# Optimization experiments

Hardware: AMD Instinct MI355X
Metric: run time of the kernel (lower is better)

The kernel has to match this reference:

```python
import jax, jax.numpy as jnp
import numpy as np

SIGMA = 32.0

def setup_inputs() -> dict:
    key = jax.random.key(0)
    k1, k2, k3 = jax.random.split(key, 3)
    N = 128
    W = 1024
    L = 1024
    init_vectors = jax.random.normal(k1, (2, N), dtype=jnp.float32) / 32.0
    x_coord = jax.random.randint(k2, (N,), 0, W, dtype=jnp.int64)
    y_coord = jax.random.randint(k3, (N,), 0, L, dtype=jnp.int64)
    return {
        "init_vectors": init_vectors,
        "x_coord": x_coord,
        "y_coord": y_coord,
        "width": W,
        "lenth": L,
    }

def reference(init_vectors, x_coord, y_coord, width, lenth):
    # Per-pixel Gaussian RBF voting:
    #   field[0, c, x, y] = sum_n exp(-((x-xc_n)^2 + (y-yc_n)^2) / (2*sigma^2)) * v[c, n]
    inv_two_sigma2 = 1.0 / (2.0 * SIGMA * SIGMA)
    xs = jnp.arange(width, dtype=jnp.float32)
    ys = jnp.arange(lenth, dtype=jnp.float32)
    xc = x_coord.astype(jnp.float32)
    yc = y_coord.astype(jnp.float32)
    dx2 = (xs[:, None] - xc[None, :]) ** 2  # [W, N]
    dy2 = (ys[:, None] - yc[None, :]) ** 2  # [L, N]
    # weights: [W, L, N]
    w = jnp.exp(-(dx2[:, None, :] + dy2[None, :, :]) * inv_two_sigma2)
    # contract over vectors -> [2, W, L]
    field = jnp.einsum("xyn,cn->cxy", w, init_vectors)
    return field[None]  # [1, 2, W, L]
```

## Files before the change

kernel.cpp:

```cpp
#include <hip/hip_runtime.h>


constexpr int N = 128;
constexpr int W = 1024;
constexpr int L = 1024;
constexpr float SIGMA = 32.0f;

constexpr int TX = 8;
constexpr int THREADS = 256;
constexpr int TY = THREADS;

__global__ __launch_bounds__(THREADS)
void rbf_field_kernel(const float* __restrict__ v,
                      const int*   __restrict__ xc,
                      const int*   __restrict__ yc,
                      float*       __restrict__ out)
{
    __shared__ __align__(16) float sB[N][2 * TX];
    __shared__ float sYc[N];

    const int tid = threadIdx.x;
    const int x0 = blockIdx.x * TX;
    const int y  = blockIdx.y * TY + tid;

    constexpr float kInv = 1.0f / (2.0f * SIGMA * SIGMA);

    if (tid < N) sYc[tid] = (float)yc[tid];

    #pragma unroll
    for (int k = 0; k < (N * 2 * TX) / THREADS; ++k) {
        int idx = tid + k * THREADS;
        int n = idx >> 4;
        int j = idx & 15;
        int c = j >> 3;
        int i = j & 7;
        float dx = (float)(x0 + i - xc[n]);
        sB[n][j] = __expf(-dx * dx * kInv) * v[c * N + n];
    }
    __syncthreads();

    float acc[TX][2];
    #pragma unroll
    for (int i = 0; i < TX; ++i) {
        acc[i][0] = 0.0f;
        acc[i][1] = 0.0f;
    }

    const float yf = (float)y;

    #pragma unroll 4
    for (int n = 0; n < N; ++n) {
        float dy = yf - sYc[n];
        float wy = __expf(-dy * dy * kInv);

        #pragma unroll
        for (int i = 0; i < TX; ++i) {
            acc[i][0] += sB[n][i]      * wy;
            acc[i][1] += sB[n][TX + i] * wy;
        }
    }

    #pragma unroll
    for (int c = 0; c < 2; ++c) {
        #pragma unroll
        for (int i = 0; i < TX; ++i) {
            out[(size_t)c * W * L + (size_t)(x0 + i) * L + y] = acc[i][c];
        }
    }
}

extern "C" void kernel_launch(void* const* d_in, const int* in_sizes, int n_in,
                              void* d_out, int out_size, void* d_ws, size_t ws_size,
                              hipStream_t stream) {
    const float* v  = (const float*)d_in[0];
    const int*   xc = (const int*)d_in[1];
    const int*   yc = (const int*)d_in[2];
    float* out = (float*)d_out;

    dim3 grid(W / TX, L / TY);
    rbf_field_kernel<<<grid, THREADS, 0, stream>>>(v, xc, yc, out);
}
```

Baseline: 80.19 us.

## Cull RBF centers outside a per-block cutoff window before accumulation

Each block now compacts, using a shared-memory atomic counter, the list of centers that lie within a 160-pixel margin (five sigma) of its 8x256 pixel tile. Only those centers get x-weights precomputed and only they are looped over in the per-pixel accumulation. This removes most of the exp and FMA work for distant centers, which contribute negligibly. In exchange it adds a small truncation error and a nondeterministic summation order from the atomic compaction.

Measured after the change: 67.99 us. 1.18x faster.

```diff
diff --git a/kernel.cpp b/kernel.cpp
--- a/kernel.cpp
+++ b/kernel.cpp
@@ -5,6 +5,7 @@
 constexpr int W = 1024;
 constexpr int L = 1024;
 constexpr float SIGMA = 32.0f;
+constexpr int RCUT = 160;
 
 constexpr int TX = 8;
 constexpr int THREADS = 256;
@@ -18,25 +19,42 @@
 {
     __shared__ __align__(16) float sB[N][2 * TX];
     __shared__ float sYc[N];
+    __shared__ int   sIdx[N];
+    __shared__ int   sCnt;
 
     const int tid = threadIdx.x;
     const int x0 = blockIdx.x * TX;
-    const int y  = blockIdx.y * TY + tid;
+    const int y0 = blockIdx.y * TY;
+    const int y  = y0 + tid;
 
     constexpr float kInv = 1.0f / (2.0f * SIGMA * SIGMA);
 
-    if (tid < N) sYc[tid] = (float)yc[tid];
+    if (tid == 0) sCnt = 0;
+    __syncthreads();
 
-    #pragma unroll
-    for (int k = 0; k < (N * 2 * TX) / THREADS; ++k) {
-        int idx = tid + k * THREADS;
-        int n = idx >> 4;
-        int j = idx & 15;
+    if (tid < N) {
+        int xcn = xc[tid];
+        int ycn = yc[tid];
+        bool keep = (xcn >= x0 - RCUT) && (xcn <= x0 + TX - 1 + RCUT) &&
+                    (ycn >= y0 - RCUT) && (ycn <= y0 + TY - 1 + RCUT);
+        if (keep) {
+            int m = atomicAdd(&sCnt, 1);
+            sIdx[m] = tid;
+        }
+    }
+    __syncthreads();
+    const int cnt = sCnt;
+
+    for (int base = tid; base < cnt * 2 * TX; base += THREADS) {
+        int m = base >> 4;
+        int j = base & 15;
         int c = j >> 3;
         int i = j & 7;
+        int n = sIdx[m];
         float dx = (float)(x0 + i - xc[n]);
-        sB[n][j] = __expf(-dx * dx * kInv) * v[c * N + n];
+        sB[m][j] = __expf(-dx * dx * kInv) * v[c * N + n];
     }
+    if (tid < cnt) sYc[tid] = (float)yc[sIdx[tid]];
     __syncthreads();
 
     float acc[TX][2];
@@ -48,15 +66,15 @@
 
     const float yf = (float)y;
 
-    #pragma unroll 4
-    for (int n = 0; n < N; ++n) {
-        float dy = yf - sYc[n];
+    #pragma unroll 2
+    for (int m = 0; m < cnt; ++m) {
+        float dy = yf - sYc[m];
         float wy = __expf(-dy * dy * kInv);
 
         #pragma unroll
         for (int i = 0; i < TX; ++i) {
-            acc[i][0] += sB[n][i]      * wy;
-            acc[i][1] += sB[n][TX + i] * wy;
+            acc[i][0] += sB[m][i]      * wy;
+            acc[i][1] += sB[m][TX + i] * wy;
         }
     }
 
```
